# Optimization experiments

Hardware: AMD Instinct MI355X
Metric: run time of the kernel (lower is better)

The kernel has to match this reference:

```python
import jax, jax.numpy as jnp
import numpy as np

B, P, N, DIM = 2, 2, 1024, 256
HEADS, DH = 8, 64
INNER = HEADS * DH
HW = 32
C = HW * HW  # conv channels = h1*h2 = 1024
LN_EPS = 1e-5
BN_EPS = 1e-5


def setup_inputs() -> dict:
    key = jax.random.key(0)
    ks = jax.random.split(key, 10)
    return {
        "x": jax.random.normal(ks[0], (B, P, N, DIM), jnp.float32),
        "ln_g": jnp.ones((DIM,), jnp.float32),
        "ln_b": jnp.zeros((DIM,), jnp.float32),
        "w_qkv": jax.random.normal(ks[1], (DIM, 3 * INNER), jnp.float32) * DIM ** -0.5,
        "w_conv1": jax.random.normal(ks[2], (C, 2), jnp.float32) * 0.7,
        "w_conv2": jax.random.normal(ks[3], (C, 2), jnp.float32) * 0.7,
        "w_1x1": jax.random.normal(ks[4], (C, C), jnp.float32) * C ** -0.5,
        "bn_g": jnp.ones((C,), jnp.float32),
        "bn_b": jnp.zeros((C,), jnp.float32),
        "bn_m": jax.random.normal(ks[5], (C,), jnp.float32) * 0.1,
        "bn_v": jax.random.uniform(ks[6], (C,), jnp.float32, minval=0.5, maxval=1.5),
        "w_out": jax.random.normal(ks[7], (INNER, DIM), jnp.float32) * INNER ** -0.5,
        "b_out": jnp.zeros((DIM,), jnp.float32),
    }


def _dw_conv_w(a, w):
    # depthwise (1,2) kernel, reflection pad right by 1 (pad value = col W-2)
    ap = jnp.concatenate([a, a[..., -2:-1]], axis=-1)
    return ap[..., :-1] * w[:, 0][None, :, None, None] + ap[..., 1:] * w[:, 1][None, :, None, None]


def _dw_conv_h(a, w):
    # depthwise (2,1) kernel, reflection pad bottom by 1 (pad value = row H-2)
    ap = jnp.concatenate([a, a[:, :, -2:-1, :]], axis=2)
    return ap[:, :, :-1, :] * w[:, 0][None, :, None, None] + ap[:, :, 1:, :] * w[:, 1][None, :, None, None]


def reference(x, ln_g, ln_b, w_qkv, w_conv1, w_conv2, w_1x1, bn_g, bn_b, bn_m, bn_v, w_out, b_out):
    b, p, n, dim = x.shape
    # LayerNorm
    mu = jnp.mean(x, axis=-1, keepdims=True)
    var = jnp.mean(jnp.square(x - mu), axis=-1, keepdims=True)
    xn = (x - mu) * jax.lax.rsqrt(var + LN_EPS) * ln_g + ln_b
    # QKV projection, split heads
    qkv = xn @ w_qkv  # (b,p,n,3*inner)
    q, k, v = jnp.split(qkv, 3, axis=-1)
    split_heads = lambda t: t.reshape(b, p, n, HEADS, DH).transpose(0, 1, 3, 2, 4)
    q, k, v = map(split_heads, (q, k, v))  # (b,p,h,n,d)
    dots = jnp.einsum('bphnd,bphmd->bphnm', q, k) * (DH ** -0.5)  # (b,p,h,n,n)
    # rearrange scores: n=(h1 w1), m=(h2 w2) -> channels (h1 h2), spatial (w1 w2)
    a = dots.reshape(b, p, HEADS, HW, HW, HW, HW)
    a = a.transpose(0, 1, 2, 3, 5, 4, 6).reshape(b * p * HEADS, C, HW, HW)
    a = _dw_conv_w(a, w_conv1)
    a = _dw_conv_h(a, w_conv2)
    # 1x1 conv (no bias) + BatchNorm (inference) + SiLU
    a = jnp.einsum('bchw,oc->bohw', a, w_1x1)
    inv = jax.lax.rsqrt(bn_v + BN_EPS)
    a = (a - bn_m[None, :, None, None]) * (inv * bn_g)[None, :, None, None] + bn_b[None, :, None, None]
    a = a * jax.nn.sigmoid(a)
    # rearrange back to (b,p,h,n,n)
    a = a.reshape(b, p, HEADS, HW, HW, HW, HW).transpose(0, 1, 2, 3, 5, 4, 6).reshape(b, p, HEADS, n, n)
    attn = jax.nn.softmax(a, axis=-1)
    out = jnp.einsum('bphnm,bphmd->bphnd', attn, v)
    out = out.transpose(0, 1, 3, 2, 4).reshape(b, p, n, INNER)
    return out @ w_out + b_out
```

## Files before the change

kernel.cpp:

```cpp
#include <hip/hip_runtime.h>
#include <hip/hip_fp16.h>


#define DEV __device__ __forceinline__

typedef __attribute__((ext_vector_type(8))) _Float16 f16x8;
typedef __attribute__((ext_vector_type(4))) float f32x4;
typedef __attribute__((ext_vector_type(8))) unsigned short u16x8;

DEV float h2f_bits(unsigned short u) { __half h; *reinterpret_cast<unsigned short*>(&h) = u; return __half2float(h); }
DEV unsigned short f2h_bits(float f) { __half h = __float2half(f); return *reinterpret_cast<unsigned short*>(&h); }

__global__ __launch_bounds__(256) void prep_kernel(
    const float* __restrict__ wqkv, const float* __restrict__ w1x1,
    const float* __restrict__ wout,
    __half* __restrict__ WQKVT, __half* __restrict__ W1X1H, __half* __restrict__ WOTT) {
  int i0 = blockIdx.x * 256 + threadIdx.x;
  int stride = gridDim.x * 256;
  for (int i = i0; i < 1536 * 256; i += stride) {
    int j = i >> 8, k = i & 255;
    WQKVT[i] = __float2half(wqkv[k * 1536 + j]);
  }
  for (int i = i0; i < 1024 * 1024; i += stride) {
    int o = i >> 10, p = i & 1023;
    int blk = p >> 5, r = p & 31, a = r >> 3, bb = r & 7;
    int h1 = (blk >> 2) * 4 + a, h2 = (blk & 3) * 8 + bb;
    W1X1H[i] = __float2half(w1x1[o * 1024 + h1 * 32 + h2]);
  }
  for (int i = i0; i < 256 * 512; i += stride) {
    int j = i >> 9, k = i & 511;
    WOTT[i] = __float2half(wout[k * 256 + j]);
  }
}

__global__ __launch_bounds__(256) void ln_kernel(const float* __restrict__ x,
    const float* __restrict__ g, const float* __restrict__ b, __half* __restrict__ XN) {
  int row = blockIdx.x;
  int tid = threadIdx.x, lane = tid & 63, wid = tid >> 6;
  float xv = x[(size_t)row * 256 + tid];
  float s = xv, q = xv * xv;
#pragma unroll
  for (int off = 32; off; off >>= 1) { s += __shfl_xor(s, off); q += __shfl_xor(q, off); }
  __shared__ float rs[4], rq[4];
  if (lane == 0) { rs[wid] = s; rq[wid] = q; }
  __syncthreads();
  s = rs[0] + rs[1] + rs[2] + rs[3];
  q = rq[0] + rq[1] + rq[2] + rq[3];
  float mu = s * (1.f / 256.f);
  float var = q * (1.f / 256.f) - mu * mu;
  float r = rsqrtf(var + 1e-5f);
  XN[(size_t)row * 256 + tid] = __float2half((xv - mu) * r * g[tid] + b[tid]);
}

template <int BM, int BN, int BK, int WGN, int FM, int FN, class Epi>
__global__ __launch_bounds__(256) void gemm_bt(
    const __half* __restrict__ A, long long aStride,
    const __half* __restrict__ B, long long bStride,
    int K, Epi epi) {
  constexpr int CPR = BK / 8;
  constexpr int NCA = (BM * BK) / (8 * 256);
  constexpr int NCB = (BN * BK) / (8 * 256);
  constexpr int KSUB = BK / 32;
  __shared__ __align__(16) __half smA[2][BM * BK];
  __shared__ __align__(16) __half smB[2][BN * BK];
  const int tid = threadIdx.x;
  const int lane = tid & 63, wid = tid >> 6;
  const int wr = wid / WGN, wc = wid % WGN;
  const int gx = gridDim.x, gxy = gridDim.x * gridDim.y;
  const int nwg = gxy * gridDim.z;
  const int b_lin = blockIdx.x + blockIdx.y * gx + blockIdx.z * gxy;
  const int logical = (b_lin & 7) * (nwg >> 3) + (b_lin >> 3);
  const int bx = logical % gx, by = (logical / gx) % gridDim.y, bz = logical / gxy;
  const int img = bz;
  const int row0 = bx * BM;
  const int col0 = by * BN;
  const __half* Ab = A + (size_t)((long long)img * aStride);
  const __half* Bb = B + (size_t)((long long)img * bStride);
  f32x4 acc[FM][FN] = {};
  const int lr = lane & 15;
  const int kq = lane >> 4;

  auto swz = [](int c, int r) -> int {
    return (CPR == 8) ? (c ^ (r & 7)) : (c ^ ((r >> 1) & 3));
  };

  const __half* pA[NCA]; int dA[NCA];
  const __half* pB[NCB]; int dB[NCB];
#pragma unroll
  for (int it = 0; it < NCA; ++it) {
    int e = it * 256 + tid, r = e / CPR, c = e % CPR;
    pA[it] = Ab + (size_t)(row0 + r) * K + swz(c, r) * 8;
    dA[it] = r * BK + c * 8;
  }
#pragma unroll
  for (int it = 0; it < NCB; ++it) {
    int e = it * 256 + tid, r = e / CPR, c = e % CPR;
    pB[it] = Bb + (size_t)(col0 + r) * K + swz(c, r) * 8;
    dB[it] = r * BK + c * 8;
  }

  auto stage = [&](int buf, int kt) {
#pragma unroll
    for (int it = 0; it < NCA; ++it)
      __builtin_amdgcn_global_load_lds(
          (const __attribute__((address_space(1))) unsigned int*)(pA[it] + kt),
          (__attribute__((address_space(3))) unsigned int*)(&smA[buf][dA[it]]),
          16, 0, 0);
#pragma unroll
    for (int it = 0; it < NCB; ++it)
      __builtin_amdgcn_global_load_lds(
          (const __attribute__((address_space(1))) unsigned int*)(pB[it] + kt),
          (__attribute__((address_space(3))) unsigned int*)(&smB[buf][dB[it]]),
          16, 0, 0);
  };

  const int NT = K / BK;
  stage(0, 0);
  __syncthreads();
  int cur = 0;
  for (int t = 0; t < NT; ++t) {
    if (t + 1 < NT) stage(cur ^ 1, (t + 1) * BK);
#pragma unroll
    for (int kk = 0; kk < KSUB; ++kk) {
      f16x8 av[FM], bv[FN];
#pragma unroll
      for (int i = 0; i < FM; ++i) {
        int row = wr * FM * 16 + i * 16 + lr;
        int ch = swz(kk * 4 + kq, lr);
        av[i] = *reinterpret_cast<const f16x8*>(&smA[cur][row * BK + ch * 8]);
      }
#pragma unroll
      for (int j = 0; j < FN; ++j) {
        int row = wc * FN * 16 + j * 16 + lr;
        int ch = swz(kk * 4 + kq, lr);
        bv[j] = *reinterpret_cast<const f16x8*>(&smB[cur][row * BK + ch * 8]);
      }
#pragma unroll
      for (int i = 0; i < FM; ++i)
#pragma unroll
        for (int j = 0; j < FN; ++j)
          acc[i][j] = __builtin_amdgcn_mfma_f32_16x16x32_f16(av[i], bv[j], acc[i][j], 0, 0, 0);
    }
    __syncthreads();
    cur ^= 1;
  }

  const int orow = row0 + wr * FM * 16 + (lane >> 4) * 4;
  const int ocol = col0 + wc * FN * 16 + lr;
#pragma unroll
  for (int i = 0; i < FM; ++i)
#pragma unroll
    for (int j = 0; j < FN; ++j)
#pragma unroll
      for (int q = 0; q < 4; ++q)
        epi.store(img, orow + i * 16 + q, ocol + j * 16, acc[i][j][q]);
}

struct EpiQKV {
  __half *Q, *K, *V;
  DEV void store(int, int t, int j, float v) const {
    int part = j >> 9, inner = j & 511;
    int h = inner >> 6, d = inner & 63;
    int bp = t >> 10, n = t & 1023;
    size_t img = (size_t)(bp * 8 + h);
    if (part == 0)       Q[(img * 1024 + n) * 64 + d] = __float2half(v * 0.125f);
    else if (part == 1)  K[(img * 1024 + n) * 64 + d] = __float2half(v);
    else                 V[(img * 64 + d) * 1024 + n] = __float2half(v);
  }
};
struct EpiPV {
  __half* O;
  DEV void store(int img, int n, int d, float v) const {
    int bp = img >> 3, h = img & 7;
    O[((size_t)(bp * 1024 + n)) * 512 + h * 64 + d] = __float2half(v);
  }
};
struct EpiOut {
  float* out; const float* bias;
  DEV void store(int, int t, int j, float v) const {
    out[(size_t)t * 256 + j] = v + bias[j];
  }
};

__global__ __launch_bounds__(512) void qkconv_kernel(
    const __half* __restrict__ Q, const __half* __restrict__ Km,
    const float* __restrict__ wc1, const float* __restrict__ wc2,
    __half* __restrict__ AC) {
  constexpr int NP = 132;
  __shared__ __align__(16) char LDS[77824];
  __half* smA = (__half*)LDS;
  __half* smB = (__half*)(LDS + 16384);
  __half* Dt  = (__half*)LDS;
  __half* T   = (__half*)(LDS + 67584);
  const int tid = threadIdx.x;
  const int lane = tid & 63, wid = tid >> 6;
  const int wr = wid >> 2, wc = wid & 3;
  const int gx = gridDim.x, gxy = gx * gridDim.y;
  const int nwg = gxy * gridDim.z;
  const int b_lin = blockIdx.x + blockIdx.y * gx + blockIdx.z * gxy;
  const int logical = (b_lin & 7) * (nwg >> 3) + (b_lin >> 3);
  const int bx = logical % gx, by = (logical / gx) % gridDim.y, bz = logical / gxy;
  const int img = bz, row0 = bx * 128, col0 = by * 256;
  const __half* Qi = Q + ((size_t)img << 16);
  const __half* Ki = Km + ((size_t)img << 16);

#pragma unroll
  for (int it = 0; it < 2; ++it) {
    int e = it * 512 + tid, r = e >> 3, c = e & 7, sc = c ^ (r & 7);
    __builtin_amdgcn_global_load_lds(
        (const __attribute__((address_space(1))) unsigned int*)(Qi + (size_t)(row0 + r) * 64 + sc * 8),
        (__attribute__((address_space(3))) unsigned int*)(smA + r * 64 + c * 8), 16, 0, 0);
  }
#pragma unroll
  for (int it = 0; it < 4; ++it) {
    int e = it * 512 + tid, r = e >> 3, c = e & 7, sc = c ^ (r & 7);
    __builtin_amdgcn_global_load_lds(
        (const __attribute__((address_space(1))) unsigned int*)(Ki + (size_t)(col0 + r) * 64 + sc * 8),
        (__attribute__((address_space(3))) unsigned int*)(smB + r * 64 + c * 8), 16, 0, 0);
  }
  __syncthreads();

  const int lr = lane & 15, kq = lane >> 4;
  f32x4 acc[4][4] = {};
#pragma unroll
  for (int kk = 0; kk < 2; ++kk) {
    const int ch = (kk * 4 + kq) ^ (lr & 7);
    f16x8 av[4], bv[4];
#pragma unroll
    for (int i = 0; i < 4; ++i)
      av[i] = *reinterpret_cast<const f16x8*>(&smA[(wr * 64 + i * 16 + lr) * 64 + ch * 8]);
#pragma unroll
    for (int j = 0; j < 4; ++j)
      bv[j] = *reinterpret_cast<const f16x8*>(&smB[(wc * 64 + j * 16 + lr) * 64 + ch * 8]);
#pragma unroll
    for (int i = 0; i < 4; ++i)
#pragma unroll
      for (int j = 0; j < 4; ++j)
        acc[i][j] = __builtin_amdgcn_mfma_f32_16x16x32_f16(av[i], bv[j], acc[i][j], 0, 0, 0);
  }
  __syncthreads();

#pragma unroll
  for (int i = 0; i < 4; ++i) {
    int n0 = wr * 64 + i * 16 + kq * 4;
#pragma unroll
    for (int j = 0; j < 4; ++j) {
      int m = wc * 64 + j * 16 + lr;
      ushort4 o4;
      o4.x = f2h_bits(acc[i][j][0]); o4.y = f2h_bits(acc[i][j][1]);
      o4.z = f2h_bits(acc[i][j][2]); o4.w = f2h_bits(acc[i][j][3]);
      *reinterpret_cast<ushort4*>(Dt + m * NP + n0) = o4;
    }
  }
  __syncthreads();

  const int w2i = tid >> 7;
  const int b_  = (tid >> 4) & 7;
  const int a_  = (tid >> 2) & 3;
  const int w1q = (tid & 3) * 8;
  const int cch = (bx * 4 + a_) * 32 + (by * 8 + b_);
  const float u0 = wc1[2 * cch], u1 = wc1[2 * cch + 1];
  const float v0 = wc2[2 * cch], v1 = wc2[2 * cch + 1];
  const int cblk = (bx * 4 + by) * 32;
  __half* ACi = AC + ((size_t)img << 20);
  const int w1o = (tid >> 2) & 31, ck = tid & 3;

  for (int pass = 0; pass < 8; ++pass) {
    const int w2 = pass * 4 + w2i;
    const int w2n = (w2 < 31) ? w2 + 1 : 30;
    const __half* r0 = Dt + (b_ * 32 + w2) * NP + a_ * 32 + w1q;
    const __half* r1 = Dt + (b_ * 32 + w2n) * NP + a_ * 32 + w1q;
    float X[9];
    {
      ushort4 x0a = *reinterpret_cast<const ushort4*>(r0);
      ushort4 x0b = *reinterpret_cast<const ushort4*>(r0 + 4);
      ushort4 x1a = *reinterpret_cast<const ushort4*>(r1);
      ushort4 x1b = *reinterpret_cast<const ushort4*>(r1 + 4);
      X[0] = u0 * h2f_bits(x0a.x) + u1 * h2f_bits(x1a.x);
      X[1] = u0 * h2f_bits(x0a.y) + u1 * h2f_bits(x1a.y);
      X[2] = u0 * h2f_bits(x0a.z) + u1 * h2f_bits(x1a.z);
      X[3] = u0 * h2f_bits(x0a.w) + u1 * h2f_bits(x1a.w);
      X[4] = u0 * h2f_bits(x0b.x) + u1 * h2f_bits(x1b.x);
      X[5] = u0 * h2f_bits(x0b.y) + u1 * h2f_bits(x1b.y);
      X[6] = u0 * h2f_bits(x0b.z) + u1 * h2f_bits(x1b.z);
      X[7] = u0 * h2f_bits(x0b.w) + u1 * h2f_bits(x1b.w);
      X[8] = u0 * __half2float(r0[8]) + u1 * __half2float(r1[8]);
    }
#pragma unroll
    for (int k = 0; k < 8; ++k) {
      float ov = (w1q + k < 31) ? (v0 * X[k] + v1 * X[k + 1])
                                : (v0 * X[7] + v1 * X[6]);
      T[(w2i * 32 + w1q + k) * 40 + a_ * 8 + b_] = __float2half(ov);
    }
    __syncthreads();
    {
      const int w2o = pass * 4 + (tid >> 7);
      u16x8 v = *reinterpret_cast<const u16x8*>(T + ((tid >> 7) * 32 + w1o) * 40 + ck * 8);
      *reinterpret_cast<u16x8*>(ACi + (size_t)(w1o * 32 + w2o) * 1024 + cblk + ck * 8) = v;
    }
    __syncthreads();
  }
}

struct Epi1x1F8 {
  __half* P;
  const float *g, *b, *m, *vv;
  DEV void finalize(int img, int ob, int cb, int lane, f32x4 (&acc)[8][4]) const {
    const int lr = lane & 15, kq = lane >> 4;
    __half* Pi = P + ((size_t)img << 20);
#pragma unroll
    for (int ih = 0; ih < 4; ++ih) {
#pragma unroll
      for (int sh = 0; sh < 2; ++sh) {
        float v[2][2][4];
        float mx = -1e30f;
#pragma unroll
        for (int di = 0; di < 2; ++di) {
          int i = ih * 2 + di;
#pragma unroll
          for (int q = 0; q < 4; ++q) {
            int o = ob + i * 16 + kq * 4 + q;
            float sc = rsqrtf(vv[o] + 1e-5f) * g[o];
            float mo = m[o], bo = b[o];
#pragma unroll
            for (int dj = 0; dj < 2; ++dj) {
              float t = (acc[i][sh * 2 + dj][q] - mo) * sc + bo;
              t = t / (1.f + __expf(-t));
              v[di][dj][q] = t;
              mx = fmaxf(mx, t);
            }
          }
        }
#pragma unroll
        for (int off = 32; off; off >>= 1) mx = fmaxf(mx, __shfl_xor(mx, off));
        float sm = 0.f;
#pragma unroll
        for (int di = 0; di < 2; ++di)
#pragma unroll
          for (int dj = 0; dj < 2; ++dj)
#pragma unroll
            for (int q = 0; q < 4; ++q) {
              float e = __expf(v[di][dj][q] - mx);
              v[di][dj][q] = e; sm += e;
            }
#pragma unroll
        for (int off = 32; off; off >>= 1) sm += __shfl_xor(sm, off);
        float inv = 1.f / sm;
#pragma unroll
        for (int di = 0; di < 2; ++di) {
          int i = ih * 2 + di;
#pragma unroll
          for (int q = 0; q < 4; ++q) {
            int o = ob + i * 16 + kq * 4 + q;
            size_t nhi = (size_t)(o >> 5) * 32;
            int mlo = (o & 31) * 32;
#pragma unroll
            for (int dj = 0; dj < 2; ++dj) {
              int s = cb + (sh * 2 + dj) * 16 + lr;
              Pi[(nhi + (s >> 5)) * 1024 + mlo + (s & 31)] = __float2half(v[di][dj][q] * inv);
            }
          }
        }
      }
    }
  }
};

template <class Epi>
__global__ __launch_bounds__(512, 1) void gemm8(
    const __half* __restrict__ A, long long aStride,
    const __half* __restrict__ B, long long bStride,
    int K, Epi epi) {
  __shared__ __align__(16) __half smA[2][256 * 32];
  __shared__ __align__(16) __half smB[2][256 * 32];
  const int tid = threadIdx.x;
  const int lane = tid & 63, wid = tid >> 6;
  const int wr = wid >> 2, wc = wid & 3;
  const int gx = gridDim.x, gxy = gx * gridDim.y;
  const int nwg = gxy * gridDim.z;
  const int b_lin = blockIdx.x + blockIdx.y * gx + blockIdx.z * gxy;
  const int logical = (b_lin & 7) * (nwg >> 3) + (b_lin >> 3);
  const int bx = logical % gx, by = (logical / gx) % gridDim.y, bz = logical / gxy;
  const int img = bz, row0 = bx * 256, col0 = by * 256;
  const __half* Ab = A + (size_t)((long long)img * aStride);
  const __half* Bb = B + (size_t)((long long)img * bStride);

  const int tau = tid & 255;
  const bool grpB = (tid >= 256);
  const __half* Mb = grpB ? Bb : Ab;
  const int rc0 = grpB ? col0 : row0;
  const int cch = tau & 3;
  const int swc = cch ^ ((tau >> 3) & 3);
  const __half* pg[4]; int dstoff[4];
#pragma unroll
  for (int s = 0; s < 4; ++s) {
    int r = (tau >> 2) + 64 * s;
    pg[s] = Mb + (size_t)(rc0 + r) * K + swc * 8;
    dstoff[s] = r * 32 + cch * 8;
  }
  __half* smDst = grpB ? &smB[0][0] : &smA[0][0];
  auto stage1 = [&](int buf, int kt, int s) {
    __builtin_amdgcn_global_load_lds(
        (const __attribute__((address_space(1))) unsigned int*)(pg[s] + kt),
        (__attribute__((address_space(3))) unsigned int*)(smDst + buf * 8192 + dstoff[s]),
        16, 0, 0);
  };

  const int lr = lane & 15, kq = lane >> 4;
  const int ch = kq ^ ((lr >> 1) & 3);
  const int aOff = (wr * 128 + lr) * 32 + ch * 8;
  const int bOff = (wc * 64 + lr) * 32 + ch * 8;
  f32x4 acc[8][4] = {};

  const int NT = K / 32;
  stage1(0, 0, 0); stage1(0, 0, 1); stage1(0, 0, 2); stage1(0, 0, 3);
  __syncthreads();
  int cur = 0;
  for (int t = 0; t < NT; ++t) {
    const int ktn = (t + 1) * 32;
    const bool pf = (t + 1) < NT;
    const __half* sA = &smA[cur][0];
    const __half* sB = &smB[cur][0];
    const int nb = cur ^ 1;
    f16x8 bv[4];
    if (pf) { stage1(nb, ktn, 0); stage1(nb, ktn, 1); }
#pragma unroll
    for (int j = 0; j < 4; ++j) bv[j] = *reinterpret_cast<const f16x8*>(&sB[bOff + j * 512]);
    {
      f16x8 a0 = *reinterpret_cast<const f16x8*>(&sA[aOff + 0 * 512]);
      f16x8 a1 = *reinterpret_cast<const f16x8*>(&sA[aOff + 1 * 512]);
      __builtin_amdgcn_s_setprio(1);
#pragma unroll
      for (int j = 0; j < 4; ++j) acc[0][j] = __builtin_amdgcn_mfma_f32_16x16x32_f16(a0, bv[j], acc[0][j], 0, 0, 0);
#pragma unroll
      for (int j = 0; j < 4; ++j) acc[1][j] = __builtin_amdgcn_mfma_f32_16x16x32_f16(a1, bv[j], acc[1][j], 0, 0, 0);
      __builtin_amdgcn_s_setprio(0);
    }
    if (pf) { stage1(nb, ktn, 2); stage1(nb, ktn, 3); }
    {
      f16x8 a0 = *reinterpret_cast<const f16x8*>(&sA[aOff + 2 * 512]);
      f16x8 a1 = *reinterpret_cast<const f16x8*>(&sA[aOff + 3 * 512]);
      __builtin_amdgcn_s_setprio(1);
#pragma unroll
      for (int j = 0; j < 4; ++j) acc[2][j] = __builtin_amdgcn_mfma_f32_16x16x32_f16(a0, bv[j], acc[2][j], 0, 0, 0);
#pragma unroll
      for (int j = 0; j < 4; ++j) acc[3][j] = __builtin_amdgcn_mfma_f32_16x16x32_f16(a1, bv[j], acc[3][j], 0, 0, 0);
      __builtin_amdgcn_s_setprio(0);
    }
    {
      f16x8 a0 = *reinterpret_cast<const f16x8*>(&sA[aOff + 4 * 512]);
      f16x8 a1 = *reinterpret_cast<const f16x8*>(&sA[aOff + 5 * 512]);
      __builtin_amdgcn_s_setprio(1);
#pragma unroll
      for (int j = 0; j < 4; ++j) acc[4][j] = __builtin_amdgcn_mfma_f32_16x16x32_f16(a0, bv[j], acc[4][j], 0, 0, 0);
#pragma unroll
      for (int j = 0; j < 4; ++j) acc[5][j] = __builtin_amdgcn_mfma_f32_16x16x32_f16(a1, bv[j], acc[5][j], 0, 0, 0);
      __builtin_amdgcn_s_setprio(0);
    }
    {
      f16x8 a0 = *reinterpret_cast<const f16x8*>(&sA[aOff + 6 * 512]);
      f16x8 a1 = *reinterpret_cast<const f16x8*>(&sA[aOff + 7 * 512]);
      __builtin_amdgcn_s_setprio(1);
#pragma unroll
      for (int j = 0; j < 4; ++j) acc[6][j] = __builtin_amdgcn_mfma_f32_16x16x32_f16(a0, bv[j], acc[6][j], 0, 0, 0);
#pragma unroll
      for (int j = 0; j < 4; ++j) acc[7][j] = __builtin_amdgcn_mfma_f32_16x16x32_f16(a1, bv[j], acc[7][j], 0, 0, 0);
      __builtin_amdgcn_s_setprio(0);
    }
    __syncthreads();
    cur ^= 1;
  }
  epi.finalize(img, row0 + wr * 128, col0 + wc * 64, lane, acc);
}

extern "C" void kernel_launch(void* const* d_in, const int* in_sizes, int n_in,
                              void* d_out, int out_size, void* d_ws, size_t ws_size,
                              hipStream_t stream) {
  const float* x     = (const float*)d_in[0];
  const float* ln_g  = (const float*)d_in[1];
  const float* ln_b  = (const float*)d_in[2];
  const float* w_qkv = (const float*)d_in[3];
  const float* wc1   = (const float*)d_in[4];
  const float* wc2   = (const float*)d_in[5];
  const float* w1x1  = (const float*)d_in[6];
  const float* bn_g  = (const float*)d_in[7];
  const float* bn_b  = (const float*)d_in[8];
  const float* bn_m  = (const float*)d_in[9];
  const float* bn_v  = (const float*)d_in[10];
  const float* w_out = (const float*)d_in[11];
  const float* b_out = (const float*)d_in[12];
  float* out = (float*)d_out;

  const size_t MB = 1024 * 1024;
  char* ws = (char*)d_ws;
  __half* Pb = (__half*)ws;
  __half* ACb = (__half*)(ws + 64 * MB);
  char* p = ws + 128 * MB;
  __half* XN    = (__half*)p; p += 2 * MB;
  __half* WQKVT = (__half*)p; p += 1536 * 256 * 2;
  __half* W1X1H = (__half*)p; p += 2 * MB;
  __half* WOTT  = (__half*)p; p += 256 * 512 * 2;
  __half* Qb    = (__half*)p; p += 4 * MB;
  __half* Kb    = (__half*)p; p += 4 * MB;
  __half* Vtb   = (__half*)p; p += 4 * MB;
  __half* Ob    = (__half*)p; p += 4 * MB;

  prep_kernel<<<2048, 256, 0, stream>>>(w_qkv, w1x1, w_out, WQKVT, W1X1H, WOTT);
  ln_kernel<<<4096, 256, 0, stream>>>(x, ln_g, ln_b, XN);

  { EpiQKV e{Qb, Kb, Vtb};
    gemm_bt<128, 128, 64, 2, 4, 4, EpiQKV><<<dim3(32, 12, 1), 256, 0, stream>>>(
        XN, 0, WQKVT, 0, 256, e); }

  qkconv_kernel<<<dim3(8, 4, 32), 512, 0, stream>>>(Qb, Kb, wc1, wc2, ACb);

  { Epi1x1F8 e{Pb, bn_g, bn_b, bn_m, bn_v};
    gemm8<Epi1x1F8><<<dim3(4, 4, 32), 512, 0, stream>>>(
        W1X1H, 0, ACb, 1 << 20, 1024, e); }

  { EpiPV e{Ob};
    gemm_bt<64, 64, 64, 2, 2, 2, EpiPV><<<dim3(16, 1, 32), 256, 0, stream>>>(
        Pb, 1 << 20, Vtb, 65536, 1024, e); }

  { EpiOut e{out, b_out};
    gemm_bt<128, 128, 64, 2, 4, 4, EpiOut><<<dim3(32, 2, 1), 256, 0, stream>>>(
        Ob, 0, WOTT, 0, 512, e); }
}
```

Baseline: 196.6 us.

## Shrink 1x1-conv GEMM tiles to 128x128 with BK=64 and retile output GEMM

The 1x1-conv GEMM with its fused BN/SiLU/softmax epilogue moves from 256x256 tiles with BK=32 and one block per CU to 128x128 tiles with BK=64. It gets a new XOR-swizzled LDS layout, a simpler staging loop, and launch bounds that allow several blocks per CU. The grid grows from 512 to 2048 blocks, which should improve latency hiding and occupancy, at the cost of more redundant operand loads. The final output projection GEMM also moves to 64x64 tiles so it launches more blocks.

```diff
diff --git a/kernel.cpp b/kernel.cpp
--- a/kernel.cpp
+++ b/kernel.cpp
@@ -302,77 +302,74 @@
   }
 }
 
-struct Epi1x1F8 {
+struct Epi1x1S {
   __half* P;
   const float *g, *b, *m, *vv;
-  DEV void finalize(int img, int ob, int cb, int lane, f32x4 (&acc)[8][4]) const {
+  DEV void finalize(int img, int ob, int cb, int lane, f32x4 (&acc)[4][2]) const {
     const int lr = lane & 15, kq = lane >> 4;
     __half* Pi = P + ((size_t)img << 20);
 #pragma unroll
-    for (int ih = 0; ih < 4; ++ih) {
-#pragma unroll
-      for (int sh = 0; sh < 2; ++sh) {
-        float v[2][2][4];
-        float mx = -1e30f;
-#pragma unroll
-        for (int di = 0; di < 2; ++di) {
-          int i = ih * 2 + di;
-#pragma unroll
-          for (int q = 0; q < 4; ++q) {
-            int o = ob + i * 16 + kq * 4 + q;
-            float sc = rsqrtf(vv[o] + 1e-5f) * g[o];
-            float mo = m[o], bo = b[o];
-#pragma unroll
-            for (int dj = 0; dj < 2; ++dj) {
-              float t = (acc[i][sh * 2 + dj][q] - mo) * sc + bo;
-              t = t / (1.f + __expf(-t));
-              v[di][dj][q] = t;
-              mx = fmaxf(mx, t);
-            }
-          }
-        }
-#pragma unroll
-        for (int off = 32; off; off >>= 1) mx = fmaxf(mx, __shfl_xor(mx, off));
-        float sm = 0.f;
-#pragma unroll
-        for (int di = 0; di < 2; ++di)
-#pragma unroll
-          for (int dj = 0; dj < 2; ++dj)
-#pragma unroll
-            for (int q = 0; q < 4; ++q) {
-              float e = __expf(v[di][dj][q] - mx);
-              v[di][dj][q] = e; sm += e;
-            }
-#pragma unroll
-        for (int off = 32; off; off >>= 1) sm += __shfl_xor(sm, off);
-        float inv = 1.f / sm;
-#pragma unroll
-        for (int di = 0; di < 2; ++di) {
-          int i = ih * 2 + di;
-#pragma unroll
-          for (int q = 0; q < 4; ++q) {
-            int o = ob + i * 16 + kq * 4 + q;
-            size_t nhi = (size_t)(o >> 5) * 32;
-            int mlo = (o & 31) * 32;
-#pragma unroll
-            for (int dj = 0; dj < 2; ++dj) {
-              int s = cb + (sh * 2 + dj) * 16 + lr;
-              Pi[(nhi + (s >> 5)) * 1024 + mlo + (s & 31)] = __float2half(v[di][dj][q] * inv);
-            }
+    for (int ih = 0; ih < 2; ++ih) {
+      float v[2][2][4];
+      float mx = -1e30f;
+#pragma unroll
+      for (int di = 0; di < 2; ++di) {
+        int i = ih * 2 + di;
+#pragma unroll
+        for (int q = 0; q < 4; ++q) {
+          int o = ob + i * 16 + kq * 4 + q;
+          float sc = rsqrtf(vv[o] + 1e-5f) * g[o];
+          float mo = m[o], bo = b[o];
+#pragma unroll
+          for (int dj = 0; dj < 2; ++dj) {
+            float t = (acc[i][dj][q] - mo) * sc + bo;
+            t = t / (1.f + __expf(-t));
+            v[di][dj][q] = t;
+            mx = fmaxf(mx, t);
           }
         }
       }
+#pragma unroll
+      for (int off = 32; off; off >>= 1) mx = fmaxf(mx, __shfl_xor(mx, off));
+      float sm = 0.f;
+#pragma unroll
+      for (int di = 0; di < 2; ++di)
+#pragma unroll
+        for (int dj = 0; dj < 2; ++dj)
+#pragma unroll
+          for (int q = 0; q < 4; ++q) {
+            float e = __expf(v[di][dj][q] - mx);
+            v[di][dj][q] = e; sm += e;
+          }
+#pragma unroll
+      for (int off = 32; off; off >>= 1) sm += __shfl_xor(sm, off);
+      float inv = 1.f / sm;
+#pragma unroll
+      for (int di = 0; di < 2; ++di) {
+        int i = ih * 2 + di;
+#pragma unroll
+        for (int q = 0; q < 4; ++q) {
+          int o = ob + i * 16 + kq * 4 + q;
+          size_t nhi = (size_t)(o >> 5) * 32;
+          int mlo = (o & 31) * 32;
+#pragma unroll
+          for (int dj = 0; dj < 2; ++dj) {
+            int s = cb + dj * 16 + lr;
+            Pi[(nhi + (s >> 5)) * 1024 + mlo + (s & 31)] = __float2half(v[di][dj][q] * inv);
+          }
+        }
+      }
     }
   }
 };
 
 template <class Epi>
-__global__ __launch_bounds__(512, 1) void gemm8(
-    const __half* __restrict__ A, long long aStride,
+__global__ __launch_bounds__(512, 4) void gemm1x1(
+    const __half* __restrict__ A,
     const __half* __restrict__ B, long long bStride,
     int K, Epi epi) {
-  __shared__ __align__(16) __half smA[2][256 * 32];
-  __shared__ __align__(16) __half smB[2][256 * 32];
+  __shared__ __align__(16) __half smA[2][128 * 64];
+  __shared__ __align__(16) __half smB[2][128 * 64];
   const int tid = threadIdx.x;
   const int lane = tid & 63, wid = tid >> 6;
   const int wr = wid >> 2, wc = wid & 3;
@@ -381,96 +378,64 @@
   const int b_lin = blockIdx.x + blockIdx.y * gx + blockIdx.z * gxy;
   const int logical = (b_lin & 7) * (nwg >> 3) + (b_lin >> 3);
   const int bx = logical % gx, by = (logical / gx) % gridDim.y, bz = logical / gxy;
-  const int img = bz, row0 = bx * 256, col0 = by * 256;
-  const __half* Ab = A + (size_t)((long long)img * aStride);
+  const int img = bz, row0 = bx * 128, col0 = by * 128;
+  const __half* Ab = A;
   const __half* Bb = B + (size_t)((long long)img * bStride);
 
-  const int tau = tid & 255;
-  const bool grpB = (tid >= 256);
-  const __half* Mb = grpB ? Bb : Ab;
-  const int rc0 = grpB ? col0 : row0;
-  const int cch = tau & 3;
-  const int swc = cch ^ ((tau >> 3) & 3);
-  const __half* pg[4]; int dstoff[4];
-#pragma unroll
-  for (int s = 0; s < 4; ++s) {
-    int r = (tau >> 2) + 64 * s;
-    pg[s] = Mb + (size_t)(rc0 + r) * K + swc * 8;
-    dstoff[s] = r * 32 + cch * 8;
-  }
-  __half* smDst = grpB ? &smB[0][0] : &smA[0][0];
-  auto stage1 = [&](int buf, int kt, int s) {
-    __builtin_amdgcn_global_load_lds(
-        (const __attribute__((address_space(1))) unsigned int*)(pg[s] + kt),
-        (__attribute__((address_space(3))) unsigned int*)(smDst + buf * 8192 + dstoff[s]),
-        16, 0, 0);
+  const __half* pA[2]; int dA[2];
+  const __half* pB[2]; int dB[2];
+#pragma unroll
+  for (int it = 0; it < 2; ++it) {
+    int e = it * 512 + tid, r = e >> 3, c = e & 7, sc = c ^ (r & 7);
+    pA[it] = Ab + (size_t)(row0 + r) * K + sc * 8;
+    pB[it] = Bb + (size_t)(col0 + r) * K + sc * 8;
+    dA[it] = dB[it] = r * 64 + c * 8;
+  }
+  auto stage = [&](int buf, int kt) {
+#pragma unroll
+    for (int it = 0; it < 2; ++it)
+      __builtin_amdgcn_global_load_lds(
+          (const __attribute__((address_space(1))) unsigned int*)(pA[it] + kt),
+          (__attribute__((address_space(3))) unsigned int*)(&smA[buf][dA[it]]),
+          16, 0, 0);
+#pragma unroll
+    for (int it = 0; it < 2; ++it)
+      __builtin_amdgcn_global_load_lds(
+          (const __attribute__((address_space(1))) unsigned int*)(pB[it] + kt),
+          (__attribute__((address_space(3))) unsigned int*)(&smB[buf][dB[it]]),
+          16, 0, 0);
   };
 
   const int lr = lane & 15, kq = lane >> 4;
-  const int ch = kq ^ ((lr >> 1) & 3);
-  const int aOff = (wr * 128 + lr) * 32 + ch * 8;
-  const int bOff = (wc * 64 + lr) * 32 + ch * 8;
-  f32x4 acc[8][4] = {};
-
-  const int NT = K / 32;
-  stage1(0, 0, 0); stage1(0, 0, 1); stage1(0, 0, 2); stage1(0, 0, 3);
+  f32x4 acc[4][2] = {};
+  const int NT = K / 64;
+  stage(0, 0);
   __syncthreads();
   int cur = 0;
   for (int t = 0; t < NT; ++t) {
-    const int ktn = (t + 1) * 32;
-    const bool pf = (t + 1) < NT;
-    const __half* sA = &smA[cur][0];
-    const __half* sB = &smB[cur][0];
-    const int nb = cur ^ 1;
-    f16x8 bv[4];
-    if (pf) { stage1(nb, ktn, 0); stage1(nb, ktn, 1); }
-#pragma unroll
-    for (int j = 0; j < 4; ++j) bv[j] = *reinterpret_cast<const f16x8*>(&sB[bOff + j * 512]);
-    {
-      f16x8 a0 = *reinterpret_cast<const f16x8*>(&sA[aOff + 0 * 512]);
-      f16x8 a1 = *reinterpret_cast<const f16x8*>(&sA[aOff + 1 * 512]);
+    if (t + 1 < NT) stage(cur ^ 1, (t + 1) * 64);
+#pragma unroll
+    for (int kk = 0; kk < 2; ++kk) {
+      const int ch = (kk * 4 + kq) ^ (lr & 7);
+      f16x8 av[4], bv[2];
+#pragma unroll
+      for (int i = 0; i < 4; ++i)
+        av[i] = *reinterpret_cast<const f16x8*>(&smA[cur][(wr * 64 + i * 16 + lr) * 64 + ch * 8]);
+#pragma unroll
+      for (int j = 0; j < 2; ++j)
+        bv[j] = *reinterpret_cast<const f16x8*>(&smB[cur][(wc * 32 + j * 16 + lr) * 64 + ch * 8]);
       __builtin_amdgcn_s_setprio(1);
 #pragma unroll
-      for (int j = 0; j < 4; ++j) acc[0][j] = __builtin_amdgcn_mfma_f32_16x16x32_f16(a0, bv[j], acc[0][j], 0, 0, 0);
-#pragma unroll
-      for (int j = 0; j < 4; ++j) acc[1][j] = __builtin_amdgcn_mfma_f32_16x16x32_f16(a1, bv[j], acc[1][j], 0, 0, 0);
-      __builtin_amdgcn_s_setprio(0);
-    }
-    if (pf) { stage1(nb, ktn, 2); stage1(nb, ktn, 3); }
-    {
-      f16x8 a0 = *reinterpret_cast<const f16x8*>(&sA[aOff + 2 * 512]);
-      f16x8 a1 = *reinterpret_cast<const f16x8*>(&sA[aOff + 3 * 512]);
-      __builtin_amdgcn_s_setprio(1);
-#pragma unroll
-      for (int j = 0; j < 4; ++j) acc[2][j] = __builtin_amdgcn_mfma_f32_16x16x32_f16(a0, bv[j], acc[2][j], 0, 0, 0);
-#pragma unroll
-      for (int j = 0; j < 4; ++j) acc[3][j] = __builtin_amdgcn_mfma_f32_16x16x32_f16(a1, bv[j], acc[3][j], 0, 0, 0);
-      __builtin_amdgcn_s_setprio(0);
-    }
-    {
-      f16x8 a0 = *reinterpret_cast<const f16x8*>(&sA[aOff + 4 * 512]);
-      f16x8 a1 = *reinterpret_cast<const f16x8*>(&sA[aOff + 5 * 512]);
-      __builtin_amdgcn_s_setprio(1);
-#pragma unroll
-      for (int j = 0; j < 4; ++j) acc[4][j] = __builtin_amdgcn_mfma_f32_16x16x32_f16(a0, bv[j], acc[4][j], 0, 0, 0);
-#pragma unroll
-      for (int j = 0; j < 4; ++j) acc[5][j] = __builtin_amdgcn_mfma_f32_16x16x32_f16(a1, bv[j], acc[5][j], 0, 0, 0);
-      __builtin_amdgcn_s_setprio(0);
-    }
-    {
-      f16x8 a0 = *reinterpret_cast<const f16x8*>(&sA[aOff + 6 * 512]);
-      f16x8 a1 = *reinterpret_cast<const f16x8*>(&sA[aOff + 7 * 512]);
-      __builtin_amdgcn_s_setprio(1);
-#pragma unroll
-      for (int j = 0; j < 4; ++j) acc[6][j] = __builtin_amdgcn_mfma_f32_16x16x32_f16(a0, bv[j], acc[6][j], 0, 0, 0);
-#pragma unroll
-      for (int j = 0; j < 4; ++j) acc[7][j] = __builtin_amdgcn_mfma_f32_16x16x32_f16(a1, bv[j], acc[7][j], 0, 0, 0);
+      for (int i = 0; i < 4; ++i)
+#pragma unroll
+        for (int j = 0; j < 2; ++j)
+          acc[i][j] = __builtin_amdgcn_mfma_f32_16x16x32_f16(av[i], bv[j], acc[i][j], 0, 0, 0);
       __builtin_amdgcn_s_setprio(0);
     }
     __syncthreads();
     cur ^= 1;
   }
-  epi.finalize(img, row0 + wr * 128, col0 + wc * 64, lane, acc);
+  epi.finalize(img, row0 + wr * 64, col0 + wc * 32, lane, acc);
 }
 
 extern "C" void kernel_launch(void* const* d_in, const int* in_sizes, int n_in,
@@ -514,15 +479,15 @@
 
   qkconv_kernel<<<dim3(8, 4, 32), 512, 0, stream>>>(Qb, Kb, wc1, wc2, ACb);
 
-  { Epi1x1F8 e{Pb, bn_g, bn_b, bn_m, bn_v};
-    gemm8<Epi1x1F8><<<dim3(4, 4, 32), 512, 0, stream>>>(
-        W1X1H, 0, ACb, 1 << 20, 1024, e); }
+  { Epi1x1S e{Pb, bn_g, bn_b, bn_m, bn_v};
+    gemm1x1<Epi1x1S><<<dim3(8, 8, 32), 512, 0, stream>>>(
+        W1X1H, ACb, 1 << 20, 1024, e); }
 
   { EpiPV e{Ob};
     gemm_bt<64, 64, 64, 2, 2, 2, EpiPV><<<dim3(16, 1, 32), 256, 0, stream>>>(
         Pb, 1 << 20, Vtb, 65536, 1024, e); }
 
   { EpiOut e{out, b_out};
-    gemm_bt<128, 128, 64, 2, 4, 4, EpiOut><<<dim3(32, 2, 1), 256, 0, stream>>>(
+    gemm_bt<64, 64, 64, 2, 2, 2, EpiOut><<<dim3(64, 4, 1), 256, 0, stream>>>(
         Ob, 0, WOTT, 0, 512, e); }
 }
```

Result: faster. 184.5 us (-6.2%).
